# Kernel optimization log

Measured on AMD Instinct MI355X. Metric: run time of the kernel, lower is better.

## Reference

```python
import jax, jax.numpy as jnp
import numpy as np

N_NODES = 100000
N_EDGES = 3200000
F_IN = 512
HIDDEN = 16
N_CLASSES = 16


def setup_inputs() -> dict:
    key = jax.random.key(0)
    k1, k2, k3, k4 = jax.random.split(key, 4)
    x = jax.random.normal(k1, (N_NODES, F_IN), dtype=jnp.float32)
    edge_index = jax.random.randint(k2, (2, N_EDGES), 0, N_NODES, dtype=jnp.int32)
    # Glorot-style init for GCN weights
    W1 = jax.random.normal(k3, (F_IN, HIDDEN), dtype=jnp.float32) * np.float32(np.sqrt(2.0 / (F_IN + HIDDEN)))
    b1 = jnp.zeros((HIDDEN,), dtype=jnp.float32)
    W2 = jax.random.normal(k4, (HIDDEN, N_CLASSES), dtype=jnp.float32) * np.float32(np.sqrt(2.0 / (HIDDEN + N_CLASSES)))
    b2 = jnp.zeros((N_CLASSES,), dtype=jnp.float32)
    return {"x": x, "W1": W1, "b1": b1, "W2": W2, "b2": b2, "edge_index": edge_index}


def _gcn_conv(x, src, dst, W, b, n_nodes):
    """PyG GCNConv: h = x @ W, then symmetric-normalized aggregation with self-loops, + bias."""
    h = x @ W  # [N, out]
    # degrees include self-loops (edge weight 1.0 everywhere)
    ones = jnp.ones(src.shape[0], dtype=h.dtype)
    deg = jax.ops.segment_sum(ones, dst, num_segments=n_nodes) + 1.0  # +1 for self-loop
    dinv = jax.lax.rsqrt(deg)  # deg >= 1, no zero guard needed
    norm = dinv[src] * dinv[dst]  # [E]
    agg = jax.ops.segment_sum(h[src] * norm[:, None], dst, num_segments=n_nodes)
    # self-loop contribution: norm_ii = 1/deg_i
    agg = agg + h * (dinv * dinv)[:, None]
    return agg + b


def reference(x, W1, b1, W2, b2, edge_index):
    src, dst = edge_index[0], edge_index[1]
    n = x.shape[0]
    h = jax.nn.relu(_gcn_conv(x, src, dst, W1, b1, n))
    # dropout is identity in eval mode
    out = _gcn_conv(h, src, dst, W2, b2, n)
    return jax.nn.log_softmax(out, axis=1)
```

## Files before the change

### kernel.cpp

```cpp
#include <hip/hip_runtime.h>
#include <hip/hip_bf16.h>
#include <math.h>

constexpr int N_NODES = 100000;
constexpr int N_EDGES = 3200000;
constexpr int F_IN    = 512;
constexpr int HID     = 16;

constexpr int NPAD = 100352;

constexpr int B_BITS = 8;
constexpr int NPB    = 1 << B_BITS;
constexpr int NBKT   = (N_NODES + NPB - 1) / NPB;
constexpr int SBLK   = 400;
constexpr int CHUNK  = N_EDGES / SBLK;
constexpr int CAP    = 10240;

typedef float f32x4 __attribute__((ext_vector_type(4)));
typedef float f32x8 __attribute__((ext_vector_type(8)));
typedef unsigned short u16x8 __attribute__((ext_vector_type(8)));
typedef short bfrag8 __attribute__((ext_vector_type(8)));

__device__ __forceinline__ unsigned short f2bf_rne(float f) {
    unsigned int u = __float_as_uint(f);
    u += 0x7FFFu + ((u >> 16) & 1u);
    return (unsigned short)(u >> 16);
}
__device__ __forceinline__ float bf2f(unsigned short u) {
    return __uint_as_float((unsigned int)u << 16);
}

__global__ __launch_bounds__(256) void prep_kernel(const float* __restrict__ W1,
                                                   unsigned short* __restrict__ w1t,
                                                   int* __restrict__ gcur,
                                                   unsigned short* __restrict__ hh_bf,
                                                   unsigned short* __restrict__ hh2_bf) {
    int i = blockIdx.x * 256 + threadIdx.x;
    if (i < F_IN * HID) {
        int k = i >> 4, n = i & 15;
        w1t[n * F_IN + k] = f2bf_rne(W1[i]);
    }
    if (i < NBKT) gcur[i] = i * CAP;
    if (i < 16) {
        hh_bf [N_NODES * 16 + i] = 0;
        hh2_bf[N_NODES * 16 + i] = 0;
    }
}

__global__ __launch_bounds__(1024) void bin_scatter_kernel(const int* __restrict__ src,
                                                           const int* __restrict__ dst,
                                                           int* __restrict__ gcur,
                                                           unsigned int* __restrict__ binned) {
    __shared__ int sdst[CHUNK];
    __shared__ int ssrc[CHUNK];
    __shared__ int cnt[NBKT];
    __shared__ int cur[NBKT];
    const int tid = threadIdx.x;
    for (int t = tid; t < NBKT; t += 1024) cnt[t] = 0;
    const int base = blockIdx.x * CHUNK;
    for (int i = tid; i < CHUNK; i += 1024) {
        sdst[i] = dst[base + i];
        ssrc[i] = src[base + i];
    }
    __syncthreads();
    for (int i = tid; i < CHUNK; i += 1024)
        atomicAdd(&cnt[sdst[i] >> B_BITS], 1);
    __syncthreads();
    for (int t = tid; t < NBKT; t += 1024)
        cur[t] = cnt[t] ? atomicAdd(&gcur[t], cnt[t]) : 0;
    __syncthreads();
    for (int i = tid; i < CHUNK; i += 1024) {
        int d = sdst[i];
        int b = d >> B_BITS;
        int pos = atomicAdd(&cur[b], 1);
        binned[pos] = ((unsigned)(d & (NPB - 1)) << 24) | (unsigned)ssrc[i];
    }
}

__global__ __launch_bounds__(1024) void csr_bucket_kernel(const unsigned int* __restrict__ binned,
                                                          const int* __restrict__ gcur,
                                                          int2* __restrict__ row2,
                                                          int* __restrict__ csr,
                                                          float* __restrict__ dinv) {
    __shared__ unsigned int eb[CAP];
    __shared__ int deg[NPB];
    __shared__ int pre[NPB];
    __shared__ int cur[NPB];
    const int tid = threadIdx.x;
    const int b = blockIdx.x;
    const int e0 = b * CAP;
    int ne = gcur[b] - e0;
    if (ne > CAP) ne = CAP;
    if (ne < 0) ne = 0;

    if (tid < NPB) deg[tid] = 0;
    for (int i = tid; i < ne; i += 1024) eb[i] = binned[e0 + i];
    __syncthreads();
    for (int i = tid; i < ne; i += 1024)
        atomicAdd(&deg[eb[i] >> 24], 1);
    __syncthreads();
    if (tid < NPB) pre[tid] = (deg[tid] + 3) & ~3;
    __syncthreads();
    for (int off = 1; off < NPB; off <<= 1) {
        int v = 0;
        if (tid < NPB && tid >= off) v = pre[tid - off];
        __syncthreads();
        if (tid < NPB) pre[tid] += v;
        __syncthreads();
    }
    if (tid < NPB) {
        int excl = (tid == 0) ? 0 : pre[tid - 1];
        int start = e0 + excl;
        cur[tid] = start;
        int node = b * NPB + tid;
        if (node < N_NODES) {
            int pd = (deg[tid] + 3) & ~3;
            row2[node] = make_int2(start, start + pd);
            dinv[node] = rsqrtf((float)deg[tid] + 1.0f);
        }
    }
    __syncthreads();
    for (int i = tid; i < ne; i += 1024) {
        unsigned int v = eb[i];
        int pos = atomicAdd(&cur[v >> 24], 1);
        csr[pos] = (int)(v & 0xFFFFFFu);
    }
    if (tid < NPB) {
        int node = b * NPB + tid;
        if (node < N_NODES) {
            int d = deg[tid];
            int pdl = (d + 3) & ~3;
            int s = e0 + ((tid == 0) ? 0 : pre[tid - 1]) + d;
            for (int q = d; q < pdl; ++q) csr[s++] = N_NODES;
        }
    }
}

__global__ __launch_bounds__(256) void gemm1_kernel(const float* __restrict__ x,
                                                    const unsigned short* __restrict__ w1t,
                                                    const float* __restrict__ b1,
                                                    const float* __restrict__ dinv,
                                                    unsigned short* __restrict__ hh_bf,
                                                    float* __restrict__ aggs1) {
    const int tid  = threadIdx.x;
    const int lane = tid & 63;
    const int wv   = tid >> 6;
    const int m    = lane & 15;
    const int quad = lane >> 4;
    const int node0 = blockIdx.x * 64 + wv * 16;

    int gm = node0 + m; if (gm >= N_NODES) gm = N_NODES - 1;
    const float* arow = x + (size_t)gm * F_IN + quad * 8;

    bfrag8 bfr[16];
    const unsigned short* wbase = w1t + m * F_IN + quad * 8;
    #pragma unroll
    for (int t = 0; t < 16; ++t)
        bfr[t] = *(const bfrag8*)(wbase + t * 32);

    f32x4 acc = {0.f, 0.f, 0.f, 0.f};
    #pragma unroll 4
    for (int t = 0; t < 16; ++t) {
        float4 lo = *(const float4*)(arow + t * 32);
        float4 hi = *(const float4*)(arow + t * 32 + 4);
        union { bfrag8 fr; __hip_bfloat162 h2[4]; } u;
        u.h2[0] = __float22bfloat162_rn(float2{lo.x, lo.y});
        u.h2[1] = __float22bfloat162_rn(float2{lo.z, lo.w});
        u.h2[2] = __float22bfloat162_rn(float2{hi.x, hi.y});
        u.h2[3] = __float22bfloat162_rn(float2{hi.z, hi.w});
        acc = __builtin_amdgcn_mfma_f32_16x16x32_bf16(u.fr, bfr[t], acc, 0, 0, 0);
    }

    const float b1j = b1[m];
    #pragma unroll
    for (int r = 0; r < 4; ++r) {
        int gn = node0 + quad * 4 + r;
        if (gn < N_NODES) {
            float dv = dinv[gn];
            float hv = acc[r] * dv;
            size_t o = (size_t)gn * 16 + m;
            hh_bf[o] = f2bf_rne(hv);
            aggs1[o] = hv * dv + b1j;
        }
    }
}

__device__ __forceinline__ f32x4 gather_rows_reduce(const unsigned short* __restrict__ tbl,
                                                    const int* __restrict__ csr,
                                                    int p, int e, int l) {
    f32x8 pA0 = {0,0,0,0,0,0,0,0}, pB0 = {0,0,0,0,0,0,0,0};
    f32x8 pA1 = {0,0,0,0,0,0,0,0}, pB1 = {0,0,0,0,0,0,0,0};
    for (; p + 4 < e; p += 8) {
        int s0 = csr[p];
        int s1 = csr[p + 4];
        const unsigned short* r0 = tbl + (s0 << 4);
        const unsigned short* r1 = tbl + (s1 << 4);
        u16x8 a0 = *(const u16x8*)(r0);
        u16x8 b0 = *(const u16x8*)(r0 + 8);
        u16x8 a1 = *(const u16x8*)(r1);
        u16x8 b1 = *(const u16x8*)(r1 + 8);
        #pragma unroll
        for (int c = 0; c < 8; ++c) {
            pA0[c] += bf2f(a0[c]); pB0[c] += bf2f(b0[c]);
            pA1[c] += bf2f(a1[c]); pB1[c] += bf2f(b1[c]);
        }
    }
    if (p < e) {
        int s0 = csr[p];
        const unsigned short* r0 = tbl + (s0 << 4);
        u16x8 a0 = *(const u16x8*)(r0);
        u16x8 b0 = *(const u16x8*)(r0 + 8);
        #pragma unroll
        for (int c = 0; c < 8; ++c) {
            pA0[c] += bf2f(a0[c]); pB0[c] += bf2f(b0[c]);
        }
    }
    f32x8 A = pA0 + pA1;
    f32x8 B = pB0 + pB1;
    const bool hi2 = (l & 2) != 0;
    f32x8 send = hi2 ? A : B;
    f32x8 keep = hi2 ? B : A;
    #pragma unroll
    for (int c = 0; c < 8; ++c) keep[c] += __shfl_xor(send[c], 2);
    const bool hi1 = (l & 1) != 0;
    f32x4 s2, k2;
    #pragma unroll
    for (int c = 0; c < 4; ++c) {
        s2[c] = hi1 ? keep[c] : keep[c + 4];
        k2[c] = hi1 ? keep[c + 4] : keep[c];
    }
    #pragma unroll
    for (int c = 0; c < 4; ++c) k2[c] += __shfl_xor(s2[c], 1);
    return k2;
}

__global__ __launch_bounds__(256) void pull1_kernel(const unsigned short* __restrict__ hh_bf,
                                                    const float* __restrict__ aggs1,
                                                    const float* __restrict__ dinv,
                                                    const int2* __restrict__ row2,
                                                    const int* __restrict__ csr,
                                                    const float* __restrict__ W2,
                                                    const float* __restrict__ b2,
                                                    unsigned short* __restrict__ hh2_bf,
                                                    float* __restrict__ aggs2) {
    __shared__ f32x4 w2s[64];
    __shared__ f32x4 b2s[4];
    const int tid = threadIdx.x;
    if (tid < 64) w2s[tid] = ((const f32x4*)W2)[tid];
    if (tid < 4)  b2s[tid] = ((const f32x4*)b2)[tid];
    __syncthreads();

    int t = blockIdx.x * 256 + tid;
    int node = t >> 2;
    int l = t & 3;
    if (node >= N_NODES) return;

    int2 re = row2[node];
    f32x4 a = gather_rows_reduce(hh_bf, csr, re.x + l, re.y, l);

    float dv = dinv[node];
    f32x4 base = *(const f32x4*)(aggs1 + ((size_t)node << 4) + (l << 2));
    float v[4];
    #pragma unroll
    for (int c = 0; c < 4; ++c) v[c] = fmaxf(base[c] + dv * a[c], 0.f);

    f32x4 h2 = {0.f, 0.f, 0.f, 0.f};
    #pragma unroll
    for (int k = 0; k < 16; ++k) {
        float vk = __shfl(v[k & 3], k >> 2, 4);
        f32x4 w = w2s[k * 4 + l];
        h2.x += vk * w.x; h2.y += vk * w.y; h2.z += vk * w.z; h2.w += vk * w.w;
    }
    f32x4 bb = b2s[l];
    ushort4 hs;
    f32x4 ag;
    float hv0 = h2.x * dv; hs.x = f2bf_rne(hv0); ag.x = hv0 * dv + bb.x;
    float hv1 = h2.y * dv; hs.y = f2bf_rne(hv1); ag.y = hv1 * dv + bb.y;
    float hv2 = h2.z * dv; hs.z = f2bf_rne(hv2); ag.z = hv2 * dv + bb.z;
    float hv3 = h2.w * dv; hs.w = f2bf_rne(hv3); ag.w = hv3 * dv + bb.w;
    size_t o = ((size_t)node << 4) + (l << 2);
    *(ushort4*)(hh2_bf + o) = hs;
    *(f32x4*)(aggs2 + o) = ag;
}

__global__ __launch_bounds__(256) void pull2_kernel(const unsigned short* __restrict__ hh2_bf,
                                                    const float* __restrict__ aggs2,
                                                    const float* __restrict__ dinv,
                                                    const int2* __restrict__ row2,
                                                    const int* __restrict__ csr,
                                                    float* __restrict__ out) {
    int t = blockIdx.x * 256 + threadIdx.x;
    int node = t >> 2;
    int l = t & 3;
    if (node >= N_NODES) return;

    int2 re = row2[node];
    f32x4 a = gather_rows_reduce(hh2_bf, csr, re.x + l, re.y, l);

    float dv = dinv[node];
    f32x4 base = *(const f32x4*)(aggs2 + ((size_t)node << 4) + (l << 2));
    f32x4 o4;
    o4.x = base.x + dv * a.x; o4.y = base.y + dv * a.y;
    o4.z = base.z + dv * a.z; o4.w = base.w + dv * a.w;

    float m = fmaxf(fmaxf(o4.x, o4.y), fmaxf(o4.z, o4.w));
    m = fmaxf(m, __shfl_xor(m, 1));
    m = fmaxf(m, __shfl_xor(m, 2));
    float s = expf(o4.x - m) + expf(o4.y - m) + expf(o4.z - m) + expf(o4.w - m);
    s += __shfl_xor(s, 1);
    s += __shfl_xor(s, 2);
    float ls = m + logf(s);
    f32x4 r;
    r.x = o4.x - ls; r.y = o4.y - ls; r.z = o4.z - ls; r.w = o4.w - ls;
    *(f32x4*)(out + ((size_t)node << 4) + (l << 2)) = r;
}

extern "C" void kernel_launch(void* const* d_in, const int* in_sizes, int n_in,
                              void* d_out, int out_size, void* d_ws, size_t ws_size,
                              hipStream_t stream) {
    const float* x    = (const float*)d_in[0];
    const float* W1   = (const float*)d_in[1];
    const float* b1   = (const float*)d_in[2];
    const float* W2   = (const float*)d_in[3];
    const float* b2   = (const float*)d_in[4];
    const int*   ei   = (const int*)d_in[5];
    const int*   src  = ei;
    const int*   dst  = ei + N_EDGES;
    float* out = (float*)d_out;

    constexpr size_t SLOTS    = (size_t)NBKT * CAP;
    constexpr size_t OFF_DINV = 512;
    constexpr size_t OFF_ROW2 = 512 + (size_t)NPAD;
    constexpr size_t OFF_CSR  = 512 + 3 * (size_t)NPAD;
    constexpr size_t OFF_HH   = OFF_CSR + SLOTS;
    constexpr size_t OFF_AG1  = OFF_HH + 800512;
    constexpr size_t OFF_HH2  = OFF_AG1 + 1600000;
    constexpr size_t OFF_AG2  = OFF_HH2 + 800512;
    constexpr size_t OFF_W1T  = OFF_AG2 + 1600000;

    int*   wsi  = (int*)d_ws;
    float* wsf  = (float*)d_ws;
    int*   gcur  = wsi;
    float* dinv  = wsf + OFF_DINV;
    int2*  row2  = (int2*)(wsi + OFF_ROW2);
    int*   csr   = wsi + OFF_CSR;
    unsigned int* binned = (unsigned int*)csr;
    unsigned short* hh_bf  = (unsigned short*)(wsi + OFF_HH);
    float*          aggs1  = wsf + OFF_AG1;
    unsigned short* hh2_bf = (unsigned short*)(wsi + OFF_HH2);
    float*          aggs2  = wsf + OFF_AG2;
    unsigned short* w1t    = (unsigned short*)(wsi + OFF_W1T);

    const int MB  = (N_NODES + 63) / 64;
    const int GB4 = (N_NODES * 4 + 255) / 256;

    prep_kernel       <<<32, 256, 0, stream>>>(W1, w1t, gcur, hh_bf, hh2_bf);
    bin_scatter_kernel<<<SBLK, 1024, 0, stream>>>(src, dst, gcur, binned);
    csr_bucket_kernel <<<NBKT, 1024, 0, stream>>>(binned, gcur, row2, csr, dinv);
    gemm1_kernel      <<<MB, 256, 0, stream>>>(x, w1t, b1, dinv, hh_bf, aggs1);
    pull1_kernel      <<<GB4, 256, 0, stream>>>(hh_bf, aggs1, dinv, row2, csr, W2, b2, hh2_bf, aggs2);
    pull2_kernel      <<<GB4, 256, 0, stream>>>(hh2_bf, aggs2, dinv, row2, csr, out);
}
```

Measured before the change: 448.2 us.

## Replace CSR pull aggregation with per-bucket shared-memory atomic accumulation

Drops building the per-node CSR (prefix scan, padded rows, scatter) and keeps only degree computation. Both aggregation passes now run one 1024-thread block per 256-node destination bucket. Each block walks that bucket's binned edges, gathers bf16 source rows, and accumulates them with float atomics into a 16 KB LDS tile, then does the epilogue. This removes the CSR construction kernel work but adds 16 LDS atomics per edge and uses only about 391 blocks, which limits parallelism.

New measurement: 1.043 ms. +132.8%, slower.

```diff
diff --git a/kernel.cpp b/kernel.cpp
--- a/kernel.cpp
+++ b/kernel.cpp
@@ -17,7 +17,6 @@
 constexpr int CAP    = 10240;
 
 typedef float f32x4 __attribute__((ext_vector_type(4)));
-typedef float f32x8 __attribute__((ext_vector_type(8)));
 typedef unsigned short u16x8 __attribute__((ext_vector_type(8)));
 typedef short bfrag8 __attribute__((ext_vector_type(8)));
 
@@ -32,19 +31,13 @@
 
 __global__ __launch_bounds__(256) void prep_kernel(const float* __restrict__ W1,
                                                    unsigned short* __restrict__ w1t,
-                                                   int* __restrict__ gcur,
-                                                   unsigned short* __restrict__ hh_bf,
-                                                   unsigned short* __restrict__ hh2_bf) {
+                                                   int* __restrict__ gcur) {
     int i = blockIdx.x * 256 + threadIdx.x;
     if (i < F_IN * HID) {
         int k = i >> 4, n = i & 15;
         w1t[n * F_IN + k] = f2bf_rne(W1[i]);
     }
     if (i < NBKT) gcur[i] = i * CAP;
-    if (i < 16) {
-        hh_bf [N_NODES * 16 + i] = 0;
-        hh2_bf[N_NODES * 16 + i] = 0;
-    }
 }
 
 __global__ __launch_bounds__(1024) void bin_scatter_kernel(const int* __restrict__ src,
@@ -77,62 +70,24 @@
     }
 }
 
-__global__ __launch_bounds__(1024) void csr_bucket_kernel(const unsigned int* __restrict__ binned,
-                                                          const int* __restrict__ gcur,
-                                                          int2* __restrict__ row2,
-                                                          int* __restrict__ csr,
-                                                          float* __restrict__ dinv) {
-    __shared__ unsigned int eb[CAP];
+__global__ __launch_bounds__(1024) void deg_kernel(const unsigned int* __restrict__ binned,
+                                                   const int* __restrict__ gcur,
+                                                   float* __restrict__ dinv) {
     __shared__ int deg[NPB];
-    __shared__ int pre[NPB];
-    __shared__ int cur[NPB];
     const int tid = threadIdx.x;
     const int b = blockIdx.x;
     const int e0 = b * CAP;
     int ne = gcur[b] - e0;
     if (ne > CAP) ne = CAP;
     if (ne < 0) ne = 0;
-
     if (tid < NPB) deg[tid] = 0;
-    for (int i = tid; i < ne; i += 1024) eb[i] = binned[e0 + i];
     __syncthreads();
     for (int i = tid; i < ne; i += 1024)
-        atomicAdd(&deg[eb[i] >> 24], 1);
-    __syncthreads();
-    if (tid < NPB) pre[tid] = (deg[tid] + 3) & ~3;
-    __syncthreads();
-    for (int off = 1; off < NPB; off <<= 1) {
-        int v = 0;
-        if (tid < NPB && tid >= off) v = pre[tid - off];
-        __syncthreads();
-        if (tid < NPB) pre[tid] += v;
-        __syncthreads();
-    }
-    if (tid < NPB) {
-        int excl = (tid == 0) ? 0 : pre[tid - 1];
-        int start = e0 + excl;
-        cur[tid] = start;
-        int node = b * NPB + tid;
-        if (node < N_NODES) {
-            int pd = (deg[tid] + 3) & ~3;
-            row2[node] = make_int2(start, start + pd);
-            dinv[node] = rsqrtf((float)deg[tid] + 1.0f);
-        }
-    }
-    __syncthreads();
-    for (int i = tid; i < ne; i += 1024) {
-        unsigned int v = eb[i];
-        int pos = atomicAdd(&cur[v >> 24], 1);
-        csr[pos] = (int)(v & 0xFFFFFFu);
-    }
+        atomicAdd(&deg[binned[e0 + i] >> 24], 1);
+    __syncthreads();
     if (tid < NPB) {
         int node = b * NPB + tid;
-        if (node < N_NODES) {
-            int d = deg[tid];
-            int pdl = (d + 3) & ~3;
-            int s = e0 + ((tid == 0) ? 0 : pre[tid - 1]) + d;
-            for (int q = d; q < pdl; ++q) csr[s++] = N_NODES;
-        }
+        if (node < N_NODES) dinv[node] = rsqrtf((float)deg[tid] + 1.0f);
     }
 }
 
@@ -185,84 +140,56 @@
     }
 }
 
-__device__ __forceinline__ f32x4 gather_rows_reduce(const unsigned short* __restrict__ tbl,
-                                                    const int* __restrict__ csr,
-                                                    int p, int e, int l) {
-    f32x8 pA0 = {0,0,0,0,0,0,0,0}, pB0 = {0,0,0,0,0,0,0,0};
-    f32x8 pA1 = {0,0,0,0,0,0,0,0}, pB1 = {0,0,0,0,0,0,0,0};
-    for (; p + 4 < e; p += 8) {
-        int s0 = csr[p];
-        int s1 = csr[p + 4];
-        const unsigned short* r0 = tbl + (s0 << 4);
-        const unsigned short* r1 = tbl + (s1 << 4);
-        u16x8 a0 = *(const u16x8*)(r0);
-        u16x8 b0 = *(const u16x8*)(r0 + 8);
-        u16x8 a1 = *(const u16x8*)(r1);
-        u16x8 b1 = *(const u16x8*)(r1 + 8);
-        #pragma unroll
-        for (int c = 0; c < 8; ++c) {
-            pA0[c] += bf2f(a0[c]); pB0[c] += bf2f(b0[c]);
-            pA1[c] += bf2f(a1[c]); pB1[c] += bf2f(b1[c]);
-        }
-    }
-    if (p < e) {
-        int s0 = csr[p];
-        const unsigned short* r0 = tbl + (s0 << 4);
-        u16x8 a0 = *(const u16x8*)(r0);
-        u16x8 b0 = *(const u16x8*)(r0 + 8);
-        #pragma unroll
-        for (int c = 0; c < 8; ++c) {
-            pA0[c] += bf2f(a0[c]); pB0[c] += bf2f(b0[c]);
-        }
-    }
-    f32x8 A = pA0 + pA1;
-    f32x8 B = pB0 + pB1;
-    const bool hi2 = (l & 2) != 0;
-    f32x8 send = hi2 ? A : B;
-    f32x8 keep = hi2 ? B : A;
-    #pragma unroll
-    for (int c = 0; c < 8; ++c) keep[c] += __shfl_xor(send[c], 2);
-    const bool hi1 = (l & 1) != 0;
-    f32x4 s2, k2;
-    #pragma unroll
-    for (int c = 0; c < 4; ++c) {
-        s2[c] = hi1 ? keep[c] : keep[c + 4];
-        k2[c] = hi1 ? keep[c + 4] : keep[c];
-    }
-    #pragma unroll
-    for (int c = 0; c < 4; ++c) k2[c] += __shfl_xor(s2[c], 1);
-    return k2;
-}
-
-__global__ __launch_bounds__(256) void pull1_kernel(const unsigned short* __restrict__ hh_bf,
+__global__ __launch_bounds__(1024) void agg1_kernel(const unsigned int* __restrict__ binned,
+                                                    const int* __restrict__ gcur,
+                                                    const unsigned short* __restrict__ hh_bf,
                                                     const float* __restrict__ aggs1,
                                                     const float* __restrict__ dinv,
-                                                    const int2* __restrict__ row2,
-                                                    const int* __restrict__ csr,
                                                     const float* __restrict__ W2,
                                                     const float* __restrict__ b2,
                                                     unsigned short* __restrict__ hh2_bf,
                                                     float* __restrict__ aggs2) {
+    __shared__ float acc[NPB * 16];
     __shared__ f32x4 w2s[64];
     __shared__ f32x4 b2s[4];
     const int tid = threadIdx.x;
+    const int b = blockIdx.x;
+    #pragma unroll
+    for (int q = 0; q < 4; ++q) acc[tid + q * 1024] = 0.f;
     if (tid < 64) w2s[tid] = ((const f32x4*)W2)[tid];
     if (tid < 4)  b2s[tid] = ((const f32x4*)b2)[tid];
     __syncthreads();
 
-    int t = blockIdx.x * 256 + tid;
-    int node = t >> 2;
-    int l = t & 3;
+    const int e0 = b * CAP;
+    int ne = gcur[b] - e0;
+    if (ne > CAP) ne = CAP;
+    if (ne < 0) ne = 0;
+    for (int i = tid; i < ne; i += 1024) {
+        unsigned int v = binned[e0 + i];
+        int ld = v >> 24;
+        int s  = (int)(v & 0xFFFFFFu);
+        const unsigned short* row = hh_bf + ((size_t)s << 4);
+        u16x8 gA = *(const u16x8*)(row);
+        u16x8 gB = *(const u16x8*)(row + 8);
+        float* ap = acc + ld * 16;
+        #pragma unroll
+        for (int c = 0; c < 8; ++c) {
+            atomicAdd(&ap[c],     bf2f(gA[c]));
+            atomicAdd(&ap[c + 8], bf2f(gB[c]));
+        }
+    }
+    __syncthreads();
+
+    int node_local = tid >> 2;
+    int l = tid & 3;
+    int node = b * NPB + node_local;
     if (node >= N_NODES) return;
-
-    int2 re = row2[node];
-    f32x4 a = gather_rows_reduce(hh_bf, csr, re.x + l, re.y, l);
-
     float dv = dinv[node];
     f32x4 base = *(const f32x4*)(aggs1 + ((size_t)node << 4) + (l << 2));
+    const float* ap = acc + node_local * 16 + l * 4;
     float v[4];
     #pragma unroll
-    for (int c = 0; c < 4; ++c) v[c] = fmaxf(base[c] + dv * a[c], 0.f);
+    for (int c = 0; c < 4; ++c) v[c] = fmaxf(base[c] + dv * ap[c], 0.f);
 
     f32x4 h2 = {0.f, 0.f, 0.f, 0.f};
     #pragma unroll
@@ -283,25 +210,49 @@
     *(f32x4*)(aggs2 + o) = ag;
 }
 
-__global__ __launch_bounds__(256) void pull2_kernel(const unsigned short* __restrict__ hh2_bf,
+__global__ __launch_bounds__(1024) void agg2_kernel(const unsigned int* __restrict__ binned,
+                                                    const int* __restrict__ gcur,
+                                                    const unsigned short* __restrict__ hh2_bf,
                                                     const float* __restrict__ aggs2,
                                                     const float* __restrict__ dinv,
-                                                    const int2* __restrict__ row2,
-                                                    const int* __restrict__ csr,
                                                     float* __restrict__ out) {
-    int t = blockIdx.x * 256 + threadIdx.x;
-    int node = t >> 2;
-    int l = t & 3;
+    __shared__ float acc[NPB * 16];
+    const int tid = threadIdx.x;
+    const int b = blockIdx.x;
+    #pragma unroll
+    for (int q = 0; q < 4; ++q) acc[tid + q * 1024] = 0.f;
+    __syncthreads();
+
+    const int e0 = b * CAP;
+    int ne = gcur[b] - e0;
+    if (ne > CAP) ne = CAP;
+    if (ne < 0) ne = 0;
+    for (int i = tid; i < ne; i += 1024) {
+        unsigned int v = binned[e0 + i];
+        int ld = v >> 24;
+        int s  = (int)(v & 0xFFFFFFu);
+        const unsigned short* row = hh2_bf + ((size_t)s << 4);
+        u16x8 gA = *(const u16x8*)(row);
+        u16x8 gB = *(const u16x8*)(row + 8);
+        float* ap = acc + ld * 16;
+        #pragma unroll
+        for (int c = 0; c < 8; ++c) {
+            atomicAdd(&ap[c],     bf2f(gA[c]));
+            atomicAdd(&ap[c + 8], bf2f(gB[c]));
+        }
+    }
+    __syncthreads();
+
+    int node_local = tid >> 2;
+    int l = tid & 3;
+    int node = b * NPB + node_local;
     if (node >= N_NODES) return;
-
-    int2 re = row2[node];
-    f32x4 a = gather_rows_reduce(hh2_bf, csr, re.x + l, re.y, l);
-
     float dv = dinv[node];
     f32x4 base = *(const f32x4*)(aggs2 + ((size_t)node << 4) + (l << 2));
+    const float* ap = acc + node_local * 16 + l * 4;
     f32x4 o4;
-    o4.x = base.x + dv * a.x; o4.y = base.y + dv * a.y;
-    o4.z = base.z + dv * a.z; o4.w = base.w + dv * a.w;
+    o4.x = base.x + dv * ap[0]; o4.y = base.y + dv * ap[1];
+    o4.z = base.z + dv * ap[2]; o4.w = base.w + dv * ap[3];
 
     float m = fmaxf(fmaxf(o4.x, o4.y), fmaxf(o4.z, o4.w));
     m = fmaxf(m, __shfl_xor(m, 1));
@@ -330,34 +281,30 @@
 
     constexpr size_t SLOTS    = (size_t)NBKT * CAP;
     constexpr size_t OFF_DINV = 512;
-    constexpr size_t OFF_ROW2 = 512 + (size_t)NPAD;
-    constexpr size_t OFF_CSR  = 512 + 3 * (size_t)NPAD;
-    constexpr size_t OFF_HH   = OFF_CSR + SLOTS;
-    constexpr size_t OFF_AG1  = OFF_HH + 800512;
+    constexpr size_t OFF_BIN  = 512 + (size_t)NPAD;
+    constexpr size_t OFF_HH   = OFF_BIN + SLOTS;
+    constexpr size_t OFF_AG1  = OFF_HH + 800000;
     constexpr size_t OFF_HH2  = OFF_AG1 + 1600000;
-    constexpr size_t OFF_AG2  = OFF_HH2 + 800512;
+    constexpr size_t OFF_AG2  = OFF_HH2 + 800000;
     constexpr size_t OFF_W1T  = OFF_AG2 + 1600000;
 
     int*   wsi  = (int*)d_ws;
     float* wsf  = (float*)d_ws;
     int*   gcur  = wsi;
     float* dinv  = wsf + OFF_DINV;
-    int2*  row2  = (int2*)(wsi + OFF_ROW2);
-    int*   csr   = wsi + OFF_CSR;
-    unsigned int* binned = (unsigned int*)csr;
+    unsigned int* binned = (unsigned int*)(wsi + OFF_BIN);
     unsigned short* hh_bf  = (unsigned short*)(wsi + OFF_HH);
     float*          aggs1  = wsf + OFF_AG1;
     unsigned short* hh2_bf = (unsigned short*)(wsi + OFF_HH2);
     float*          aggs2  = wsf + OFF_AG2;
     unsigned short* w1t    = (unsigned short*)(wsi + OFF_W1T);
 
-    const int MB  = (N_NODES + 63) / 64;
-    const int GB4 = (N_NODES * 4 + 255) / 256;
-
-    prep_kernel       <<<32, 256, 0, stream>>>(W1, w1t, gcur, hh_bf, hh2_bf);
+    const int MB = (N_NODES + 63) / 64;
+
+    prep_kernel       <<<32, 256, 0, stream>>>(W1, w1t, gcur);
     bin_scatter_kernel<<<SBLK, 1024, 0, stream>>>(src, dst, gcur, binned);
-    csr_bucket_kernel <<<NBKT, 1024, 0, stream>>>(binned, gcur, row2, csr, dinv);
+    deg_kernel        <<<NBKT, 1024, 0, stream>>>(binned, gcur, dinv);
     gemm1_kernel      <<<MB, 256, 0, stream>>>(x, w1t, b1, dinv, hh_bf, aggs1);
-    pull1_kernel      <<<GB4, 256, 0, stream>>>(hh_bf, aggs1, dinv, row2, csr, W2, b2, hh2_bf, aggs2);
-    pull2_kernel      <<<GB4, 256, 0, stream>>>(hh2_bf, aggs2, dinv, row2, csr, out);
-}
+    agg1_kernel       <<<NBKT, 1024, 0, stream>>>(binned, gcur, hh_bf, aggs1, dinv, W2, b2, hh2_bf, aggs2);
+    agg2_kernel       <<<NBKT, 1024, 0, stream>>>(binned, gcur, hh2_bf, aggs2, dinv, out);
+}
```
